# Performance work log

Measured on AMD Instinct MI355X. Metric: run time of the kernel, lower is better.

The kernel has to match this reference:

```python
import jax, jax.numpy as jnp
import numpy as np

B, T, D, H, W = 2, 16, 64, 64, 64
MAX_GROWTH = 0.0  # max_growth_rate init kwarg

def _ln(x, g, b):
    m = x.mean(-1, keepdims=True)
    v = x.var(-1, keepdims=True)
    return (x - m) * jax.lax.rsqrt(v + 1e-5) * g + b

def _pscan(A, X):
    # linear recurrence h_t = A_t*h_{t-1} + X_t via Blelchlo-style associative scan over axis 1
    def comb(l, r):
        a1, x1 = l
        a2, x2 = r
        return a1 * a2, a2 * x1 + x2
    return jax.lax.associative_scan(comb, (A, X), axis=1)[1]

def setup_inputs() -> dict:
    key = jax.random.key(0)
    ks = jax.random.split(key, 20)
    n = lambda k, s, sc=1.0: jax.random.normal(k, s, dtype=jnp.float32) * sc
    inp = dict(
        x_re=n(ks[0], (B, T, D, H, W)), x_im=n(ks[1], (B, T, D, H, W)),
        h_re=n(ks[2], (B * H * W, 1, D)), h_im=n(ks[3], (B * H * W, 1, D)),
        flux_re=n(ks[4], (B, D)), flux_im=n(ks[5], (B, D)),
        dt_seq=0.01 + 0.1 * jax.random.uniform(ks[6], (B, T), dtype=jnp.float32),
        g_s=jnp.ones(2 * D, jnp.float32), b_s=jnp.zeros(2 * D, jnp.float32),
        Wc=n(ks[7], (3, 3, 2 * D, 2 * D), 1.0 / np.sqrt(9 * 2 * D)), bc=jnp.zeros(2 * D, jnp.float32),
        g_t=jnp.ones(2 * D, jnp.float32), b_t=jnp.zeros(2 * D, jnp.float32),
        E_re=n(ks[8], (D, D), 1.0 / np.sqrt(D)), E_im=n(ks[9], (D, D), 1.0 / np.sqrt(D)),
        Dec_re=n(ks[10], (D, D), 1.0 / np.sqrt(D)), Dec_im=n(ks[11], (D, D), 1.0 / np.sqrt(D)),
        lam_flux_raw=jnp.zeros(D, jnp.float32),
        Wsrc_re=n(ks[12], (D, D), 1.0 / np.sqrt(D)), Wsrc_im=n(ks[13], (D, D), 1.0 / np.sqrt(D)),
        w_gate=n(ks[14], (D,)), b_gate=jnp.zeros(D, jnp.float32),
        lam_re_raw=jnp.ones(D, jnp.float32), lam_im=n(ks[15], (D,)),
        W1=n(ks[16], (2 * D, 8 * D), 1.0 / np.sqrt(2 * D)), b1=jnp.zeros(8 * D, jnp.float32),
        W2=n(ks[17], (8 * D, 2 * D), 1.0 / np.sqrt(8 * D)), b2=jnp.zeros(2 * D, jnp.float32),
    )
    return inp

def _forward(x_re, x_im, h_re, h_im, flux_re, flux_im, dt_seq, g_s, b_s, Wc, bc, g_t, b_t,
             E_re, E_im, Dec_re, Dec_im, lam_flux_raw, Wsrc_re, Wsrc_im, w_gate, b_gate,
             lam_re_raw, lam_im, W1, b1, W2, b2):
    # channel-last complex field (B,T,H,W,D)
    x = jnp.moveaxis(x_re, 2, -1) + 1j * jnp.moveaxis(x_im, 2, -1)
    # --- spatial residual branch: LN -> Clifford(= real 2D conv on [re;im] channels) ---
    xr = jnp.concatenate([x.real, x.imag], -1)  # (B,T,H,W,2D)
    xn = _ln(xr, g_s, b_s).reshape(B * T, H, W, 2 * D)
    xs = jax.lax.conv_general_dilated(xn, Wc, (1, 1), 'SAME',
                                      dimension_numbers=('NHWC', 'HWIO', 'NHWC')) + bc
    xs = xs.reshape(B, T, H, W, 2 * D)
    x = x + (xs[..., :D] + 1j * xs[..., D:])
    # --- eigen-basis encode ---
    x_eig = jnp.einsum('bthwd,de->bthwe', x, E_re + 1j * E_im)
    x_mean = x_eig.mean((2, 3))  # (B,T,D)
    # --- flux tracker scan ---
    lam_f = jax.nn.softplus(lam_flux_raw)
    A_flux = jnp.exp(-lam_f * dt_seq[..., None])  # (B,T,D) real decay
    flux = _pscan(A_flux.astype(x_mean.dtype), x_mean * dt_seq[..., None])
    flux = flux + (flux_re + 1j * flux_im)[:, None, :] * jnp.cumprod(A_flux, axis=1)
    source = jnp.einsum('btd,de->bte', flux, Wsrc_re + 1j * Wsrc_im)
    gate = jax.nn.sigmoid(flux.real * w_gate + b_gate)  # real gate in [0,1]
    flux_out = flux[:, -1]
    ge = gate[:, :, None, None, :]
    forcing = x_eig * ge + source[:, :, None, None, :] * (1.0 - ge)
    # --- temporal propagator (exact exponential integrator) ---
    lam = (MAX_GROWTH - jax.nn.softplus(lam_re_raw)) + 1j * lam_im  # Re(lam) <= max_growth_rate
    op_decay = jnp.exp(lam * dt_seq[..., None])            # (B,T,D)
    op_forcing = (op_decay - 1.0) / lam
    u = forcing * op_forcing[:, :, None, None, :]          # (B,T,H,W,D)
    h_prev = (h_re + 1j * h_im).reshape(B, H, W, D)
    u = u.at[:, 0].add(h_prev * op_decay[:, 0][:, None, None, :])
    A_full = jnp.broadcast_to(op_decay[:, :, None, None, :], u.shape)
    u_out = _pscan(A_full, u)                              # (B,T,H,W,D)
    h_out = u_out[:, -1].reshape(B * H * W, 1, D)
    # --- decode + temporal LN/FFN residual ---
    decoded = jnp.einsum('bthwd,de->bthwe', u_out, Dec_re + 1j * Dec_im)
    dn = _ln(jnp.concatenate([decoded.real, decoded.imag], -1), g_t, b_t)
    h1 = jax.nn.gelu(jnp.einsum('bthwc,cf->bthwf', dn, W1) + b1)
    d2 = jnp.einsum('bthwf,fc->bthwc', h1, W2) + b2
    delta = d2[..., :D] + 1j * d2[..., D:]
    z = x + decoded + delta
    return z, h_out, flux_out

def reference(x_re, x_im, h_re, h_im, flux_re, flux_im, dt_seq, g_s, b_s, Wc, bc, g_t, b_t,
              E_re, E_im, Dec_re, Dec_im, lam_flux_raw, Wsrc_re, Wsrc_im, w_gate, b_gate,
              lam_re_raw, lam_im, W1, b1, W2, b2):
    z, h_out, flux_out = _forward(x_re, x_im, h_re, h_im, flux_re, flux_im, dt_seq, g_s, b_s,
                                  Wc, bc, g_t, b_t, E_re, E_im, Dec_re, Dec_im, lam_flux_raw,
                                  Wsrc_re, Wsrc_im, w_gate, b_gate, lam_re_raw, lam_im,
                                  W1, b1, W2, b2)
    # complex outputs returned as real/imag stacked on last axis
    return (jnp.stack([z.real, z.imag], -1),
            jnp.stack([h_out.real, h_out.imag], -1),
            jnp.stack([flux_out.real, flux_out.imag], -1))
```

## Files before the change

### kernel.cpp

```cpp
#include <hip/hip_runtime.h>
#include <hip/hip_bf16.h>


typedef __hip_bfloat16 bf16;
typedef __attribute__((ext_vector_type(8))) short bhalf8;
typedef __attribute__((ext_vector_type(4))) float floatx4;

#define DEV __device__ __forceinline__

DEV float b2f(const bf16 x) { return __bfloat162float(x); }
DEV bf16  f2b(float x)      { return __float2bfloat16(x); }
DEV unsigned short f2bu(float x) { bf16 h = f2b(x); return *(unsigned short*)&h; }
DEV float bu2f(unsigned short u) { unsigned int t = ((unsigned int)u) << 16; return *(float*)&t; }
DEV float softplusf(float x){ return x > 20.f ? x : log1pf(expf(x)); }
DEV float geluf(float x) {
    float v = x * fmaf(x * x, 0.10294324f, 2.30220819f);
    float e = __builtin_amdgcn_exp2f(-v);
    return x * __builtin_amdgcn_rcpf(1.f + e);
}

static constexpr int B_ = 2, T_ = 16, D_ = 64, HW = 4096;
static constexpr int NPIX = B_ * T_ * HW;
static constexpr long long N1 = (long long)NPIX * 128;

static constexpr long long BUFA  = 0;
static constexpr long long XUBF  = N1;
static constexpr long long DECBF = N1 + N1 / 2;
static constexpr long long XNBF  = 2 * N1;
static constexpr long long XCBF  = 2 * N1 + N1 / 2;
static constexpr long long XMEAN = 3 * N1;
static constexpr long long TABS  = XMEAN + 4096;
static constexpr long long FLAGO = TABS + 14336;
static constexpr long long WCP   = FLAGO + 64;
static constexpr long long W1P   = WCP + 73728;
static constexpr long long W2P   = W1P + 32768;
static constexpr long long WEP   = W2P + 32768;
static constexpr long long WDP   = WEP + 8192;

static constexpr long long ZOUT = 0;
static constexpr long long HOUT = 16777216;
static constexpr long long FOUT = 17825792;

DEV float ld(const void* p, long long i, bool bf) {
    if (bf) return b2f(((const bf16*)p)[i]);
    return ((const float*)p)[i];
}

__global__ void k_detect(const unsigned short* __restrict__ x, float* __restrict__ ws) {
    int lane = threadIdx.x;
    int cnt = 0;
    for (int i = lane; i < 256; i += 64) {
        int e = (x[i] >> 7) & 0xFF;
        cnt += (e >= 100 && e <= 140) ? 1 : 0;
    }
    for (int m = 1; m < 64; m <<= 1) cnt += __shfl_xor(cnt, m, 64);
    if (lane == 0) ws[FLAGO] = (cnt >= 224) ? 1.f : 0.f;
}

__global__ void k_convert(const void* Wc, const void* W1, const void* W2,
                          const void* Er, const void* Ei, const void* Dr, const void* Di,
                          float* ws) {
    bool bf = ws[FLAGO] != 0.f;
    int i = blockIdx.x * 256 + threadIdx.x;
    unsigned short* wcp = (unsigned short*)(ws + WCP);
    unsigned short* w1p = (unsigned short*)(ws + W1P);
    unsigned short* w2p = (unsigned short*)(ws + W2P);
    unsigned short* wep = (unsigned short*)(ws + WEP);
    unsigned short* wdp = (unsigned short*)(ws + WDP);
    if (i < 147456) {
        int j = i & 7, lane = (i >> 3) & 63, nt = (i >> 9) & 7, kc = (i >> 12) & 3, tap = i >> 14;
        int ic = kc * 32 + ((lane >> 4) << 3) + j, oc = nt * 16 + (lane & 15);
        wcp[i] = f2bu(ld(Wc, tap * 16384 + ic * 128 + oc, bf)); return;
    } i -= 147456;
    if (i < 65536) {
        int j = i & 7, lane = (i >> 3) & 63, nt = (i >> 9) & 31, kc = i >> 14;
        int ic = kc * 32 + ((lane >> 4) << 3) + j, oc = nt * 16 + (lane & 15);
        w1p[i] = f2bu(ld(W1, ic * 512 + oc, bf)); return;
    } i -= 65536;
    if (i < 65536) {
        int j = i & 7, lane = (i >> 3) & 63, nt = (i >> 9) & 7, kc = i >> 12;
        int ic = kc * 32 + ((lane >> 4) << 3) + j, oc = nt * 16 + (lane & 15);
        w2p[i] = f2bu(ld(W2, ic * 128 + oc, bf)); return;
    } i -= 65536;
    if (i < 16384) {
        int j = i & 7, lane = (i >> 3) & 63, nt = (i >> 9) & 7, kc = i >> 12;
        int k = kc * 32 + ((lane >> 4) << 3) + j, n = nt * 16 + (lane & 15);
        float v;
        if (k < 64) v = (n < 64) ? ld(Er, k * 64 + n, bf) : ld(Ei, k * 64 + (n - 64), bf);
        else        v = (n < 64) ? -ld(Ei, (k - 64) * 64 + n, bf) : ld(Er, (k - 64) * 64 + (n - 64), bf);
        wep[i] = f2bu(v); return;
    } i -= 16384;
    if (i < 16384) {
        int j = i & 7, lane = (i >> 3) & 63, nt = (i >> 9) & 7, kc = i >> 12;
        int k = kc * 32 + ((lane >> 4) << 3) + j, n = nt * 16 + (lane & 15);
        float v;
        if (k < 64) v = (n < 64) ? ld(Dr, k * 64 + n, bf) : ld(Di, k * 64 + (n - 64), bf);
        else        v = (n < 64) ? -ld(Di, (k - 64) * 64 + n, bf) : ld(Dr, (k - 64) * 64 + (n - 64), bf);
        wdp[i] = f2bu(v); return;
    }
}

__global__ __launch_bounds__(256) void kA_ln(const void* __restrict__ xre,
                                             const void* __restrict__ xim,
                                             const void* __restrict__ gs,
                                             const void* __restrict__ bs,
                                             float* __restrict__ ws) {
    __shared__ unsigned short sr[64][72] __attribute__((aligned(16)));
    __shared__ unsigned short si[64][72] __attribute__((aligned(16)));
    __shared__ float red[2][4][64];
    __shared__ float mv[64], rv[64], gb[256];
    bool bf = ws[FLAGO] != 0.f;
    int blk = blockIdx.x;
    int bt = blk >> 6;
    int px0 = (blk & 63) * 64;
    int tid = threadIdx.x;
    gb[tid] = (tid < 128) ? ld(gs, tid, bf) : ld(bs, tid - 128, bf);
    if (bf) {
        const unsigned short* xr16 = (const unsigned short*)xre;
        const unsigned short* xi16 = (const unsigned short*)xim;
        for (int l = tid; l < 1024; l += 256) {
            int a = l >> 9, dd = (l >> 3) & 63, ck = l & 7;
            long long src = (long long)bt * 262144 + (long long)dd * 4096 + px0 + ck * 8;
            bhalf8 v = *(const bhalf8*)&(a ? xi16 : xr16)[src];
            *(bhalf8*)&(a ? si : sr)[dd][ck * 8] = v;
        }
    } else {
        for (int l = tid; l < 8192; l += 256) {
            int a = l >> 12, dd = (l >> 6) & 63, px = l & 63;
            float v = ((const float*)(a ? xim : xre))[(long long)bt * 262144 + (long long)dd * 4096 + px0 + px];
            (a ? si : sr)[dd][px] = f2bu(v);
        }
    }
    __syncthreads();
    int px = tid & 63, part = tid >> 6;
    float s = 0.f, ss = 0.f;
    for (int d = part * 16; d < part * 16 + 16; d++) {
        float r = bu2f(sr[d][px]), q = bu2f(si[d][px]);
        s += r + q; ss += r * r + q * q;
    }
    red[0][part][px] = s; red[1][part][px] = ss;
    __syncthreads();
    if (tid < 64) {
        float S  = red[0][0][tid] + red[0][1][tid] + red[0][2][tid] + red[0][3][tid];
        float SS = red[1][0][tid] + red[1][1][tid] + red[1][2][tid] + red[1][3][tid];
        float m = S * (1.f / 128.f);
        mv[tid] = m;
        rv[tid] = rsqrtf(SS * (1.f / 128.f) - m * m + 1e-5f);
    }
    __syncthreads();
    unsigned short* xcb = (unsigned short*)(ws + XCBF);
    unsigned short* xnb = (unsigned short*)(ws + XNBF);
    long long pbase = ((long long)bt * 4096 + px0) * 128;
    for (int l = tid; l < 8192; l += 256) {
        int p2 = l >> 7, ch = l & 127, d = ch & 63;
        unsigned short raw = (ch < 64 ? sr : si)[d][p2];
        float v = bu2f(raw);
        xcb[pbase + p2 * 128 + ch] = raw;
        xnb[pbase + p2 * 128 + ch] = f2bu((v - mv[p2]) * rv[p2] * gb[ch] + gb[128 + ch]);
    }
}

__global__ __launch_bounds__(256) void kB_conv(const void* __restrict__ bc,
                                               float* __restrict__ ws) {
    __shared__ unsigned short xt[3][64][136] __attribute__((aligned(16)));
    bool bf = ws[FLAGO] != 0.f;
    int blk = blockIdx.x, bt = blk >> 6, h = blk & 63;
    int tid = threadIdx.x, lane = tid & 63, wv = tid >> 6;
    int m16 = lane & 15, quad = lane >> 4;
    const unsigned short* xnb = (const unsigned short*)(ws + XNBF);
    const unsigned short* wcp = (const unsigned short*)(ws + WCP);
    bhalf8 zero8 = {0, 0, 0, 0, 0, 0, 0, 0};
    for (int l = tid; l < 3072; l += 256) {
        int r = l >> 10, rem = l & 1023, col = rem >> 4, ck = rem & 15;
        int hr = h - 1 + r;
        bhalf8 v = zero8;
        if (hr >= 0 && hr < 64)
            v = *(const bhalf8*)&xnb[(((long long)bt * 4096 + hr * 64 + col) << 7) + ck * 8];
        *(bhalf8*)&xt[r][col][ck * 8] = v;
    }
    __syncthreads();
    floatx4 acc[4][2];
    #pragma unroll
    for (int mt = 0; mt < 4; mt++)
        #pragma unroll
        for (int nt = 0; nt < 2; nt++)
            acc[mt][nt] = (floatx4){0.f, 0.f, 0.f, 0.f};
    for (int tap = 0; tap < 9; tap++) {
        int dy = tap / 3, dx = tap - dy * 3;
        #pragma unroll
        for (int kc = 0; kc < 4; kc++) {
            bhalf8 bfr[2];
            #pragma unroll
            for (int nt = 0; nt < 2; nt++)
                bfr[nt] = *(const bhalf8*)&wcp[((((tap * 4 + kc) * 8) + (wv * 2 + nt)) * 64 + lane) * 8];
            #pragma unroll
            for (int mt = 0; mt < 4; mt++) {
                int col = mt * 16 + m16 + dx - 1;
                bhalf8 af = zero8;
                if (col >= 0 && col < 64)
                    af = *(const bhalf8*)&xt[dy][col][kc * 32 + quad * 8];
                acc[mt][0] = __builtin_amdgcn_mfma_f32_16x16x32_bf16(af, bfr[0], acc[mt][0], 0, 0, 0);
                acc[mt][1] = __builtin_amdgcn_mfma_f32_16x16x32_bf16(af, bfr[1], acc[mt][1], 0, 0, 0);
            }
        }
    }
    const unsigned short* xcb = (const unsigned short*)(ws + XCBF);
    unsigned short* xub = (unsigned short*)(ws + XUBF);
    #pragma unroll
    for (int nt = 0; nt < 2; nt++) {
        int n = wv * 32 + nt * 16 + m16;
        float bcv = ld(bc, n, bf);
        #pragma unroll
        for (int mt = 0; mt < 4; mt++)
            #pragma unroll
            for (int r = 0; r < 4; r++) {
                int m = mt * 16 + quad * 4 + r;
                long long p = (long long)bt * 4096 + h * 64 + m;
                xub[p * 128 + n] = f2bu(acc[mt][nt][r] + bu2f(xcb[p * 128 + n]) + bcv);
            }
    }
}

__global__ __launch_bounds__(256) void kC_eig(float* __restrict__ ws) {
    __shared__ unsigned short At[64][136] __attribute__((aligned(16)));
    int blk = blockIdx.x, bt = blk >> 6;
    long long px0 = (long long)blk * 64;
    int tid = threadIdx.x, lane = tid & 63, wv = tid >> 6;
    int m16 = lane & 15, quad = lane >> 4;
    const unsigned short* xub = (const unsigned short*)(ws + XUBF);
    for (int l = tid; l < 1024; l += 256) {
        int p2 = l >> 4, ck = l & 15;
        *(bhalf8*)&At[p2][ck * 8] = *(const bhalf8*)&xub[(px0 + p2) * 128 + ck * 8];
    }
    __syncthreads();
    const unsigned short* wep = (const unsigned short*)(ws + WEP);
    floatx4 acc[4][2];
    #pragma unroll
    for (int mt = 0; mt < 4; mt++)
        #pragma unroll
        for (int nt = 0; nt < 2; nt++)
            acc[mt][nt] = (floatx4){0.f, 0.f, 0.f, 0.f};
    #pragma unroll
    for (int kc = 0; kc < 4; kc++) {
        bhalf8 bfr[2];
        #pragma unroll
        for (int nt = 0; nt < 2; nt++)
            bfr[nt] = *(const bhalf8*)&wep[(((kc * 8) + wv * 2 + nt) * 64 + lane) * 8];
        #pragma unroll
        for (int mt = 0; mt < 4; mt++) {
            bhalf8 af = *(const bhalf8*)&At[mt * 16 + m16][kc * 32 + quad * 8];
            acc[mt][0] = __builtin_amdgcn_mfma_f32_16x16x32_bf16(af, bfr[0], acc[mt][0], 0, 0, 0);
            acc[mt][1] = __builtin_amdgcn_mfma_f32_16x16x32_bf16(af, bfr[1], acc[mt][1], 0, 0, 0);
        }
    }
    unsigned short* xeb = (unsigned short*)(ws + BUFA);
    #pragma unroll
    for (int nt = 0; nt < 2; nt++) {
        int n = wv * 32 + nt * 16 + m16;
        float part = 0.f;
        #pragma unroll
        for (int mt = 0; mt < 4; mt++)
            #pragma unroll
            for (int r = 0; r < 4; r++) {
                int m = mt * 16 + quad * 4 + r;
                xeb[(px0 + m) * 128 + n] = f2bu(acc[mt][nt][r]);
                part += acc[mt][nt][r];
            }
        part += __shfl_xor(part, 16, 64);
        part += __shfl_xor(part, 32, 64);
        if (quad == 0) atomicAdd(ws + XMEAN + bt * 128 + n, part);
    }
}

__global__ __launch_bounds__(256) void kD_flux(const void* __restrict__ fxr, const void* __restrict__ fxi,
                                               const void* __restrict__ dtseq, const void* __restrict__ lamflux,
                                               const void* __restrict__ Wsr, const void* __restrict__ Wsi,
                                               const void* __restrict__ wgate, const void* __restrict__ bgate,
                                               const void* __restrict__ lamreraw, const void* __restrict__ lamim,
                                               float* __restrict__ ws, void* __restrict__ outv) {
    bool bfo = ws[FLAGO] != 0.f;
    int b = blockIdx.x;
    int tid = threadIdx.x;
    int d = tid & 63, g = tid >> 6;
    __shared__ float fr[64], fi[64], psr[4][64], psi[4][64];
    float lam_f = softplusf(ld(lamflux, d, bfo));
    float lre = -softplusf(ld(lamreraw, d, bfo));
    float lim = ld(lamim, d, bfo);
    float cr = 0.f, ci = 0.f;
    if (g == 0) { cr = ld(fxr, b * 64 + d, bfo); ci = ld(fxi, b * 64 + d, bfo); }
    float* tabs = ws + TABS;
    const float* xmean = ws + XMEAN;
    for (int t = 0; t < 16; t++) {
        float dt = ld(dtseq, b * 16 + t, bfo);
        int idx = b * 1024 + t * 64 + d;
        if (g == 0) {
            float A = expf(-lam_f * dt);
            float xr = xmean[(b * 16 + t) * 128 + d]      * (1.f / 4096.f) * dt;
            float xq = xmean[(b * 16 + t) * 128 + 64 + d] * (1.f / 4096.f) * dt;
            cr = A * cr + xr; ci = A * ci + xq;
            fr[d] = cr; fi[d] = ci;
        }
        __syncthreads();
        {
            float pr = 0.f, pi = 0.f;
            #pragma unroll
            for (int k = 0; k < 16; k++) {
                int d2 = g * 16 + k;
                float wr = ld(Wsr, d2 * 64 + d, bfo), wi = ld(Wsi, d2 * 64 + d, bfo);
                pr += fr[d2] * wr - fi[d2] * wi;
                pi += fr[d2] * wi + fi[d2] * wr;
            }
            psr[g][d] = pr; psi[g][d] = pi;
        }
        if (g == 1) {
            float od  = expf(lre * dt);
            float odr = od * cosf(lim * dt);
            float odi = od * sinf(lim * dt);
            tabs[3 * 2048 + idx] = odr; tabs[4 * 2048 + idx] = odi;
            float den = lre * lre + lim * lim;
            float tr = odr - 1.f;
            tabs[5 * 2048 + idx] = (tr * lre + odi * lim) / den;
            tabs[6 * 2048 + idx] = (odi * lre - tr * lim) / den;
        }
        __syncthreads();
        if (g == 0) {
            float sr = psr[0][d] + psr[1][d] + psr[2][d] + psr[3][d];
            float si2 = psi[0][d] + psi[1][d] + psi[2][d] + psi[3][d];
            tabs[1 * 2048 + idx] = sr; tabs[2 * 2048 + idx] = si2;
            tabs[0 * 2048 + idx] = 1.f / (1.f + expf(-(cr * ld(wgate, d, bfo) + ld(bgate, d, bfo))));
            if (t == 15) {
                if (bfo) {
                    bf16* ob = (bf16*)outv;
                    ob[FOUT + (b * 64 + d) * 2]     = f2b(cr);
                    ob[FOUT + (b * 64 + d) * 2 + 1] = f2b(ci);
                } else {
                    float* of = (float*)outv;
                    of[FOUT + (b * 64 + d) * 2]     = cr;
                    of[FOUT + (b * 64 + d) * 2 + 1] = ci;
                }
            }
        }
    }
}

__global__ __launch_bounds__(256) void kE_scan(const void* __restrict__ hre,
                                               const void* __restrict__ him,
                                               float* __restrict__ ws, void* __restrict__ outv) {
    __shared__ float tab[7][16][64];
    bool bfo = ws[FLAGO] != 0.f;
    long long G = (long long)blockIdx.x * 256 + threadIdx.x;
    int d = threadIdx.x & 63;
    int pix = (int)((G >> 6) & 4095);
    int b = (int)(G >> 18);
    const float* tabs = ws + TABS;
    for (int l = threadIdx.x; l < 7 * 1024; l += 256) {
        int a = l >> 10, idx = l & 1023;
        ((float*)tab)[l] = tabs[a * 2048 + b * 1024 + idx];
    }
    __syncthreads();
    long long hidx = ((long long)b * 4096 + pix) * 64 + d;
    float cr = ld(hre, hidx, bfo), ci = ld(him, hidx, bfo);
    const unsigned short* xe = (const unsigned short*)(ws + BUFA);
    unsigned short* ub = (unsigned short*)(ws + XCBF);
    for (int t = 0; t < 16; t++) {
        long long base = ((long long)((b * 16 + t) * 4096 + pix)) * 128 + d;
        float xr = bu2f(xe[base]), xi = bu2f(xe[base + 64]);
        float gt = tab[0][t][d], sr = tab[1][t][d], si = tab[2][t][d];
        float odr = tab[3][t][d], odi = tab[4][t][d];
        float ofr = tab[5][t][d], ofi = tab[6][t][d];
        float fre = xr * gt + sr * (1.f - gt);
        float fim = xi * gt + si * (1.f - gt);
        float ure = fre * ofr - fim * ofi;
        float uim = fre * ofi + fim * ofr;
        float ncr = odr * cr - odi * ci + ure;
        float nci = odr * ci + odi * cr + uim;
        cr = ncr; ci = nci;
        ub[base] = f2bu(cr); ub[base + 64] = f2bu(ci);
    }
    if (bfo) {
        __hip_bfloat162 hv; hv.x = f2b(cr); hv.y = f2b(ci);
        ((__hip_bfloat162*)((bf16*)outv + HOUT))[hidx] = hv;
    } else {
        float2 hv; hv.x = cr; hv.y = ci;
        ((float2*)((float*)outv + HOUT))[hidx] = hv;
    }
}

__global__ __launch_bounds__(256) void kF1_dec(const void* __restrict__ gt_,
                                               const void* __restrict__ bt_,
                                               float* __restrict__ ws) {
    __shared__ unsigned short At[64][136] __attribute__((aligned(16)));
    __shared__ float Ct[64][132];
    __shared__ float mv[64], rv[64], gbt[256];
    bool bf = ws[FLAGO] != 0.f;
    long long px0 = (long long)blockIdx.x * 64;
    int tid = threadIdx.x, lane = tid & 63, wv = tid >> 6;
    int m16 = lane & 15, quad = lane >> 4;
    gbt[tid] = (tid < 128) ? ld(gt_, tid, bf) : ld(bt_, tid - 128, bf);
    const unsigned short* uo = (const unsigned short*)(ws + XCBF);
    for (int l = tid; l < 1024; l += 256) {
        int p2 = l >> 4, ck = l & 15;
        *(bhalf8*)&At[p2][ck * 8] = *(const bhalf8*)&uo[(px0 + p2) * 128 + ck * 8];
    }
    __syncthreads();
    const unsigned short* wdp = (const unsigned short*)(ws + WDP);
    floatx4 acc[4][2];
    #pragma unroll
    for (int mt = 0; mt < 4; mt++)
        #pragma unroll
        for (int nt = 0; nt < 2; nt++)
            acc[mt][nt] = (floatx4){0.f, 0.f, 0.f, 0.f};
    #pragma unroll
    for (int kc = 0; kc < 4; kc++) {
        bhalf8 bfr[2];
        #pragma unroll
        for (int nt = 0; nt < 2; nt++)
            bfr[nt] = *(const bhalf8*)&wdp[(((kc * 8) + wv * 2 + nt) * 64 + lane) * 8];
        #pragma unroll
        for (int mt = 0; mt < 4; mt++) {
            bhalf8 af = *(const bhalf8*)&At[mt * 16 + m16][kc * 32 + quad * 8];
            acc[mt][0] = __builtin_amdgcn_mfma_f32_16x16x32_bf16(af, bfr[0], acc[mt][0], 0, 0, 0);
            acc[mt][1] = __builtin_amdgcn_mfma_f32_16x16x32_bf16(af, bfr[1], acc[mt][1], 0, 0, 0);
        }
    }
    #pragma unroll
    for (int nt = 0; nt < 2; nt++) {
        int n = wv * 32 + nt * 16 + m16;
        #pragma unroll
        for (int mt = 0; mt < 4; mt++)
            #pragma unroll
            for (int r = 0; r < 4; r++)
                Ct[mt * 16 + quad * 4 + r][n] = acc[mt][nt][r];
    }
    __syncthreads();
    if (tid < 64) {
        float s = 0.f, ss = 0.f;
        for (int ch = 0; ch < 128; ch++) { float v = Ct[tid][ch]; s += v; ss += v * v; }
        float m = s * (1.f / 128.f);
        mv[tid] = m;
        rv[tid] = rsqrtf(ss * (1.f / 128.f) - m * m + 1e-5f);
    }
    __syncthreads();
    unsigned short* decb = (unsigned short*)(ws + DECBF);
    unsigned short* dnb  = (unsigned short*)(ws + XNBF);
    for (int l = tid; l < 8192; l += 256) {
        int p2 = l >> 7, ch = l & 127;
        float v = Ct[p2][ch];
        decb[(px0 + p2) * 128 + ch] = f2bu(v);
        dnb [(px0 + p2) * 128 + ch] = f2bu((v - mv[p2]) * rv[p2] * gbt[ch] + gbt[128 + ch]);
    }
}

__global__ __launch_bounds__(256, 5) void kMLP(const void* __restrict__ b1v,
                                               const void* __restrict__ b2v,
                                               float* __restrict__ ws, void* __restrict__ outv) {
    __shared__ unsigned short A1[32][136] __attribute__((aligned(16)));
    __shared__ unsigned short h1f[8][2][64][8] __attribute__((aligned(16)));
    __shared__ float gb2[128];
    bool bf = ws[FLAGO] != 0.f;
    long long px0 = (long long)blockIdx.x * 32;
    int tid = threadIdx.x, lane = tid & 63, wv = tid >> 6;
    int m16 = lane & 15, quad = lane >> 4;
    const unsigned short* dnb = (const unsigned short*)(ws + XNBF);
    if (tid < 128) gb2[tid] = ld(b2v, tid, bf);
    for (int l = tid; l < 512; l += 256) {
        int p2 = l >> 4, ck = l & 15;
        *(bhalf8*)&A1[p2][ck * 8] = *(const bhalf8*)&dnb[(px0 + p2) * 128 + ck * 8];
    }
    __syncthreads();
    const unsigned short* w1p = (const unsigned short*)(ws + W1P);
    const unsigned short* w2p = (const unsigned short*)(ws + W2P);
    floatx4 acc2[2][2];
    #pragma unroll
    for (int mt = 0; mt < 2; mt++)
        #pragma unroll
        for (int nt = 0; nt < 2; nt++)
            acc2[mt][nt] = (floatx4){0.f, 0.f, 0.f, 0.f};

    #pragma unroll
    for (int ph = 0; ph < 2; ph++) {
        floatx4 acc1[2][4];
        #pragma unroll
        for (int mt = 0; mt < 2; mt++)
            #pragma unroll
            for (int nt4 = 0; nt4 < 4; nt4++)
                acc1[mt][nt4] = (floatx4){0.f, 0.f, 0.f, 0.f};
        #pragma unroll
        for (int kc = 0; kc < 4; kc++) {
            bhalf8 af0 = *(const bhalf8*)&A1[m16][kc * 32 + quad * 8];
            bhalf8 af1 = *(const bhalf8*)&A1[16 + m16][kc * 32 + quad * 8];
            #pragma unroll
            for (int nt4 = 0; nt4 < 4; nt4++) {
                int nt = ph * 4 + nt4;
                bhalf8 bfr = *(const bhalf8*)&w1p[(((kc * 32) + wv * 8 + nt) * 64 + lane) * 8];
                acc1[0][nt4] = __builtin_amdgcn_mfma_f32_16x16x32_bf16(af0, bfr, acc1[0][nt4], 0, 0, 0);
                acc1[1][nt4] = __builtin_amdgcn_mfma_f32_16x16x32_bf16(af1, bfr, acc1[1][nt4], 0, 0, 0);
            }
        }
        #pragma unroll
        for (int nt4 = 0; nt4 < 4; nt4++) {
            int nt = ph * 4 + nt4;
            int n = (wv * 8 + nt) * 16 + m16;
            float b1f = ld(b1v, n, bf);
            int qp = ((nt * 2) + (m16 >> 3)) & 3;
            int slot = wv * 2 + (nt4 >> 1);
            int j = m16 & 7;
            #pragma unroll
            for (int mt = 0; mt < 2; mt++)
                #pragma unroll
                for (int r = 0; r < 4; r++)
                    h1f[slot][mt][qp * 16 + quad * 4 + r][j] =
                        f2bu(geluf(acc1[mt][nt4][r] + b1f));
        }
        __syncthreads();
        #pragma unroll
        for (int s = 0; s < 8; s++) {
            int kc2g = (s >> 1) * 4 + (s & 1) + ph * 2;
            bhalf8 a0 = *(const bhalf8*)&h1f[s][0][lane][0];
            bhalf8 a1 = *(const bhalf8*)&h1f[s][1][lane][0];
            #pragma unroll
            for (int nt = 0; nt < 2; nt++) {
                bhalf8 bfr = *(const bhalf8*)&w2p[(((kc2g * 8) + wv * 2 + nt) * 64 + lane) * 8];
                acc2[0][nt] = __builtin_amdgcn_mfma_f32_16x16x32_bf16(a0, bfr, acc2[0][nt], 0, 0, 0);
                acc2[1][nt] = __builtin_amdgcn_mfma_f32_16x16x32_bf16(a1, bfr, acc2[1][nt], 0, 0, 0);
            }
        }
        if (ph == 0) __syncthreads();
    }
    #pragma unroll
    for (int nt = 0; nt < 2; nt++) {
        int n = wv * 32 + nt * 16 + m16;
        #pragma unroll
        for (int mt = 0; mt < 2; mt++)
            #pragma unroll
            for (int r = 0; r < 4; r++)
                A1[mt * 16 + quad * 4 + r][n] = f2bu(acc2[mt][nt][r]);
    }
    __syncthreads();
    {
        const unsigned short* decb = (const unsigned short*)(ws + DECBF);
        const unsigned short* xub  = (const unsigned short*)(ws + XUBF);
        int pxl = tid >> 3, dc = (tid & 7) * 8;
        long long p = px0 + pxl;
        bhalf8 cre = *(const bhalf8*)&A1[pxl][dc];
        bhalf8 cim = *(const bhalf8*)&A1[pxl][64 + dc];
        bhalf8 xr8 = *(const bhalf8*)&xub[p * 128 + dc];
        bhalf8 xi8 = *(const bhalf8*)&xub[p * 128 + 64 + dc];
        bhalf8 dr8 = *(const bhalf8*)&decb[p * 128 + dc];
        bhalf8 di8 = *(const bhalf8*)&decb[p * 128 + 64 + dc];
        float zr[8], zi[8];
        #pragma unroll
        for (int k = 0; k < 8; k++) {
            zr[k] = bu2f((unsigned short)cre[k]) + gb2[dc + k]
                  + bu2f((unsigned short)xr8[k]) + bu2f((unsigned short)dr8[k]);
            zi[k] = bu2f((unsigned short)cim[k]) + gb2[64 + dc + k]
                  + bu2f((unsigned short)xi8[k]) + bu2f((unsigned short)di8[k]);
        }
        if (bf) {
            unsigned short o[16];
            #pragma unroll
            for (int k = 0; k < 8; k++) { o[2 * k] = f2bu(zr[k]); o[2 * k + 1] = f2bu(zi[k]); }
            unsigned short* ob = (unsigned short*)outv;
            *(bhalf8*)&ob[ZOUT + p * 128 + 2 * dc]     = *(bhalf8*)&o[0];
            *(bhalf8*)&ob[ZOUT + p * 128 + 2 * dc + 8] = *(bhalf8*)&o[8];
        } else {
            float* of = (float*)outv + ZOUT + p * 128 + 2 * dc;
            #pragma unroll
            for (int k = 0; k < 8; k++) { of[2 * k] = zr[k]; of[2 * k + 1] = zi[k]; }
        }
    }
}

extern "C" void kernel_launch(void* const* d_in, const int* in_sizes, int n_in,
                              void* d_out, int out_size, void* d_ws, size_t ws_size,
                              hipStream_t stream) {
    const void* x_re  = d_in[0];
    const void* x_im  = d_in[1];
    const void* h_re  = d_in[2];
    const void* h_im  = d_in[3];
    const void* fl_re = d_in[4];
    const void* fl_im = d_in[5];
    const void* dtseq = d_in[6];
    const void* g_s   = d_in[7];
    const void* b_s   = d_in[8];
    const void* Wc    = d_in[9];
    const void* bc    = d_in[10];
    const void* g_t   = d_in[11];
    const void* b_t   = d_in[12];
    const void* E_re  = d_in[13];
    const void* E_im  = d_in[14];
    const void* De_re = d_in[15];
    const void* De_im = d_in[16];
    const void* lamfl = d_in[17];
    const void* Ws_re = d_in[18];
    const void* Ws_im = d_in[19];
    const void* wgate = d_in[20];
    const void* bgate = d_in[21];
    const void* lamrr = d_in[22];
    const void* lamim = d_in[23];
    const void* W1    = d_in[24];
    const void* b1    = d_in[25];
    const void* W2    = d_in[26];
    const void* b2    = d_in[27];
    float* ws = (float*)d_ws;

    hipMemsetAsync((char*)d_ws + XMEAN * sizeof(float), 0, 4096 * sizeof(float), stream);
    k_detect<<<1, 64, 0, stream>>>((const unsigned short*)x_re, ws);
    k_convert<<<1216, 256, 0, stream>>>(Wc, W1, W2, E_re, E_im, De_re, De_im, ws);
    kA_ln<<<2048, 256, 0, stream>>>(x_re, x_im, g_s, b_s, ws);
    kB_conv<<<2048, 256, 0, stream>>>(bc, ws);
    kC_eig<<<2048, 256, 0, stream>>>(ws);
    kD_flux<<<2, 256, 0, stream>>>(fl_re, fl_im, dtseq, lamfl, Ws_re, Ws_im,
                                   wgate, bgate, lamrr, lamim, ws, d_out);
    kE_scan<<<2048, 256, 0, stream>>>(h_re, h_im, ws, d_out);
    kF1_dec<<<2048, 256, 0, stream>>>(g_t, b_t, ws);
    kMLP<<<4096, 256, 0, stream>>>(b1, b2, ws, d_out);
}
```

Before: 450.3 us.

## Fuse eig projection into conv kernel and decoder+LN into MLP kernel

Folds the E-projection GEMM into the conv kernel, reusing the conv output tile from shared memory rather than reloading it from global memory. The decoder GEMM and its LayerNorm move into the MLP kernel, so the decoded and normalized intermediates are no longer written to and read back from global memory. The scan kernel now processes two channels per thread with packed loads and stores, which halves its grid. In exchange, shared-memory pressure rises: the MLP kernel aliases buffers in a pool and needs extra barriers, and its occupancy hint drops from 5 to 4.

```diff
diff --git a/kernel.cpp b/kernel.cpp
--- a/kernel.cpp
+++ b/kernel.cpp
@@ -204,6 +204,8 @@
             }
         }
     }
+    __syncthreads();
+    unsigned short (*At)[136] = (unsigned short(*)[136])&xt[0][0][0];
     const unsigned short* xcb = (const unsigned short*)(ws + XCBF);
     unsigned short* xub = (unsigned short*)(ws + XUBF);
     #pragma unroll
@@ -216,30 +218,20 @@
             for (int r = 0; r < 4; r++) {
                 int m = mt * 16 + quad * 4 + r;
                 long long p = (long long)bt * 4096 + h * 64 + m;
-                xub[p * 128 + n] = f2bu(acc[mt][nt][r] + bu2f(xcb[p * 128 + n]) + bcv);
-            }
-    }
-}
-
-__global__ __launch_bounds__(256) void kC_eig(float* __restrict__ ws) {
-    __shared__ unsigned short At[64][136] __attribute__((aligned(16)));
-    int blk = blockIdx.x, bt = blk >> 6;
+                unsigned short u = f2bu(acc[mt][nt][r] + bu2f(xcb[p * 128 + n]) + bcv);
+                xub[p * 128 + n] = u;
+                At[m][n] = u;
+            }
+    }
+    __syncthreads();
+    const unsigned short* wep = (const unsigned short*)(ws + WEP);
     long long px0 = (long long)blk * 64;
-    int tid = threadIdx.x, lane = tid & 63, wv = tid >> 6;
-    int m16 = lane & 15, quad = lane >> 4;
-    const unsigned short* xub = (const unsigned short*)(ws + XUBF);
-    for (int l = tid; l < 1024; l += 256) {
-        int p2 = l >> 4, ck = l & 15;
-        *(bhalf8*)&At[p2][ck * 8] = *(const bhalf8*)&xub[(px0 + p2) * 128 + ck * 8];
-    }
-    __syncthreads();
-    const unsigned short* wep = (const unsigned short*)(ws + WEP);
-    floatx4 acc[4][2];
+    floatx4 acce[4][2];
     #pragma unroll
     for (int mt = 0; mt < 4; mt++)
         #pragma unroll
         for (int nt = 0; nt < 2; nt++)
-            acc[mt][nt] = (floatx4){0.f, 0.f, 0.f, 0.f};
+            acce[mt][nt] = (floatx4){0.f, 0.f, 0.f, 0.f};
     #pragma unroll
     for (int kc = 0; kc < 4; kc++) {
         bhalf8 bfr[2];
@@ -249,8 +241,8 @@
         #pragma unroll
         for (int mt = 0; mt < 4; mt++) {
             bhalf8 af = *(const bhalf8*)&At[mt * 16 + m16][kc * 32 + quad * 8];
-            acc[mt][0] = __builtin_amdgcn_mfma_f32_16x16x32_bf16(af, bfr[0], acc[mt][0], 0, 0, 0);
-            acc[mt][1] = __builtin_amdgcn_mfma_f32_16x16x32_bf16(af, bfr[1], acc[mt][1], 0, 0, 0);
+            acce[mt][0] = __builtin_amdgcn_mfma_f32_16x16x32_bf16(af, bfr[0], acce[mt][0], 0, 0, 0);
+            acce[mt][1] = __builtin_amdgcn_mfma_f32_16x16x32_bf16(af, bfr[1], acce[mt][1], 0, 0, 0);
         }
     }
     unsigned short* xeb = (unsigned short*)(ws + BUFA);
@@ -263,8 +255,8 @@
             #pragma unroll
             for (int r = 0; r < 4; r++) {
                 int m = mt * 16 + quad * 4 + r;
-                xeb[(px0 + m) * 128 + n] = f2bu(acc[mt][nt][r]);
-                part += acc[mt][nt][r];
+                xeb[(px0 + m) * 128 + n] = f2bu(acce[mt][nt][r]);
+                part += acce[mt][nt][r];
             }
         part += __shfl_xor(part, 16, 64);
         part += __shfl_xor(part, 32, 64);
@@ -348,125 +340,160 @@
                                                float* __restrict__ ws, void* __restrict__ outv) {
     __shared__ float tab[7][16][64];
     bool bfo = ws[FLAGO] != 0.f;
-    long long G = (long long)blockIdx.x * 256 + threadIdx.x;
-    int d = threadIdx.x & 63;
-    int pix = (int)((G >> 6) & 4095);
-    int b = (int)(G >> 18);
+    int tid = threadIdx.x;
+    long long G = (long long)blockIdx.x * 256 + tid;
+    int d0 = (int)(G & 31) * 2;
+    int pixg = (int)(G >> 5);
+    int pix = pixg & 4095;
+    int b = pixg >> 12;
     const float* tabs = ws + TABS;
-    for (int l = threadIdx.x; l < 7 * 1024; l += 256) {
+    for (int l = tid; l < 7 * 1024; l += 256) {
         int a = l >> 10, idx = l & 1023;
         ((float*)tab)[l] = tabs[a * 2048 + b * 1024 + idx];
     }
     __syncthreads();
-    long long hidx = ((long long)b * 4096 + pix) * 64 + d;
-    float cr = ld(hre, hidx, bfo), ci = ld(him, hidx, bfo);
+    long long hidx = ((long long)b * 4096 + pix) * 64 + d0;
+    float cr0, ci0, cr1, ci1;
+    if (bfo) {
+        unsigned int r2 = *(const unsigned int*)&((const unsigned short*)hre)[hidx];
+        unsigned int i2 = *(const unsigned int*)&((const unsigned short*)him)[hidx];
+        cr0 = bu2f((unsigned short)(r2 & 0xffff)); cr1 = bu2f((unsigned short)(r2 >> 16));
+        ci0 = bu2f((unsigned short)(i2 & 0xffff)); ci1 = bu2f((unsigned short)(i2 >> 16));
+    } else {
+        float2 r2 = *(const float2*)((const float*)hre + hidx);
+        float2 i2 = *(const float2*)((const float*)him + hidx);
+        cr0 = r2.x; cr1 = r2.y; ci0 = i2.x; ci1 = i2.y;
+    }
     const unsigned short* xe = (const unsigned short*)(ws + BUFA);
     unsigned short* ub = (unsigned short*)(ws + XCBF);
     for (int t = 0; t < 16; t++) {
-        long long base = ((long long)((b * 16 + t) * 4096 + pix)) * 128 + d;
-        float xr = bu2f(xe[base]), xi = bu2f(xe[base + 64]);
-        float gt = tab[0][t][d], sr = tab[1][t][d], si = tab[2][t][d];
-        float odr = tab[3][t][d], odi = tab[4][t][d];
-        float ofr = tab[5][t][d], ofi = tab[6][t][d];
-        float fre = xr * gt + sr * (1.f - gt);
-        float fim = xi * gt + si * (1.f - gt);
-        float ure = fre * ofr - fim * ofi;
-        float uim = fre * ofi + fim * ofr;
-        float ncr = odr * cr - odi * ci + ure;
-        float nci = odr * ci + odi * cr + uim;
-        cr = ncr; ci = nci;
-        ub[base] = f2bu(cr); ub[base + 64] = f2bu(ci);
+        long long base = ((long long)((b * 16 + t) * 4096 + pix)) * 128 + d0;
+        unsigned int xr2 = *(const unsigned int*)&xe[base];
+        unsigned int xi2 = *(const unsigned int*)&xe[base + 64];
+        float2 gt2  = *(const float2*)&tab[0][t][d0];
+        float2 sr2  = *(const float2*)&tab[1][t][d0];
+        float2 si2  = *(const float2*)&tab[2][t][d0];
+        float2 odr2 = *(const float2*)&tab[3][t][d0];
+        float2 odi2 = *(const float2*)&tab[4][t][d0];
+        float2 ofr2 = *(const float2*)&tab[5][t][d0];
+        float2 ofi2 = *(const float2*)&tab[6][t][d0];
+        {
+            float xr = bu2f((unsigned short)(xr2 & 0xffff));
+            float xi = bu2f((unsigned short)(xi2 & 0xffff));
+            float fre = xr * gt2.x + sr2.x * (1.f - gt2.x);
+            float fim = xi * gt2.x + si2.x * (1.f - gt2.x);
+            float ure = fre * ofr2.x - fim * ofi2.x;
+            float uim = fre * ofi2.x + fim * ofr2.x;
+            float n0 = odr2.x * cr0 - odi2.x * ci0 + ure;
+            float n1 = odr2.x * ci0 + odi2.x * cr0 + uim;
+            cr0 = n0; ci0 = n1;
+        }
+        {
+            float xr = bu2f((unsigned short)(xr2 >> 16));
+            float xi = bu2f((unsigned short)(xi2 >> 16));
+            float fre = xr * gt2.y + sr2.y * (1.f - gt2.y);
+            float fim = xi * gt2.y + si2.y * (1.f - gt2.y);
+            float ure = fre * ofr2.y - fim * ofi2.y;
+            float uim = fre * ofi2.y + fim * ofr2.y;
+            float n0 = odr2.y * cr1 - odi2.y * ci1 + ure;
+            float n1 = odr2.y * ci1 + odi2.y * cr1 + uim;
+            cr1 = n0; ci1 = n1;
+        }
+        *(unsigned int*)&ub[base]      = (unsigned int)f2bu(cr0) | ((unsigned int)f2bu(cr1) << 16);
+        *(unsigned int*)&ub[base + 64] = (unsigned int)f2bu(ci0) | ((unsigned int)f2bu(ci1) << 16);
     }
     if (bfo) {
-        __hip_bfloat162 hv; hv.x = f2b(cr); hv.y = f2b(ci);
-        ((__hip_bfloat162*)((bf16*)outv + HOUT))[hidx] = hv;
+        uint2 hv;
+        hv.x = (unsigned int)f2bu(cr0) | ((unsigned int)f2bu(ci0) << 16);
+        hv.y = (unsigned int)f2bu(cr1) | ((unsigned int)f2bu(ci1) << 16);
+        *(uint2*)((unsigned short*)outv + HOUT + 2 * hidx) = hv;
     } else {
-        float2 hv; hv.x = cr; hv.y = ci;
-        ((float2*)((float*)outv + HOUT))[hidx] = hv;
-    }
-}
-
-__global__ __launch_bounds__(256) void kF1_dec(const void* __restrict__ gt_,
+        float4 hv; hv.x = cr0; hv.y = ci0; hv.z = cr1; hv.w = ci1;
+        *(float4*)((float*)outv + HOUT + 2 * hidx) = hv;
+    }
+}
+
+__global__ __launch_bounds__(256, 4) void kMLP(const void* __restrict__ gt_,
                                                const void* __restrict__ bt_,
-                                               float* __restrict__ ws) {
-    __shared__ unsigned short At[64][136] __attribute__((aligned(16)));
-    __shared__ float Ct[64][132];
-    __shared__ float mv[64], rv[64], gbt[256];
-    bool bf = ws[FLAGO] != 0.f;
-    long long px0 = (long long)blockIdx.x * 64;
-    int tid = threadIdx.x, lane = tid & 63, wv = tid >> 6;
-    int m16 = lane & 15, quad = lane >> 4;
-    gbt[tid] = (tid < 128) ? ld(gt_, tid, bf) : ld(bt_, tid - 128, bf);
-    const unsigned short* uo = (const unsigned short*)(ws + XCBF);
-    for (int l = tid; l < 1024; l += 256) {
-        int p2 = l >> 4, ck = l & 15;
-        *(bhalf8*)&At[p2][ck * 8] = *(const bhalf8*)&uo[(px0 + p2) * 128 + ck * 8];
-    }
-    __syncthreads();
-    const unsigned short* wdp = (const unsigned short*)(ws + WDP);
-    floatx4 acc[4][2];
-    #pragma unroll
-    for (int mt = 0; mt < 4; mt++)
-        #pragma unroll
-        for (int nt = 0; nt < 2; nt++)
-            acc[mt][nt] = (floatx4){0.f, 0.f, 0.f, 0.f};
-    #pragma unroll
-    for (int kc = 0; kc < 4; kc++) {
-        bhalf8 bfr[2];
-        #pragma unroll
-        for (int nt = 0; nt < 2; nt++)
-            bfr[nt] = *(const bhalf8*)&wdp[(((kc * 8) + wv * 2 + nt) * 64 + lane) * 8];
-        #pragma unroll
-        for (int mt = 0; mt < 4; mt++) {
-            bhalf8 af = *(const bhalf8*)&At[mt * 16 + m16][kc * 32 + quad * 8];
-            acc[mt][0] = __builtin_amdgcn_mfma_f32_16x16x32_bf16(af, bfr[0], acc[mt][0], 0, 0, 0);
-            acc[mt][1] = __builtin_amdgcn_mfma_f32_16x16x32_bf16(af, bfr[1], acc[mt][1], 0, 0, 0);
-        }
-    }
-    #pragma unroll
-    for (int nt = 0; nt < 2; nt++) {
-        int n = wv * 32 + nt * 16 + m16;
-        #pragma unroll
-        for (int mt = 0; mt < 4; mt++)
-            #pragma unroll
-            for (int r = 0; r < 4; r++)
-                Ct[mt * 16 + quad * 4 + r][n] = acc[mt][nt][r];
-    }
-    __syncthreads();
-    if (tid < 64) {
-        float s = 0.f, ss = 0.f;
-        for (int ch = 0; ch < 128; ch++) { float v = Ct[tid][ch]; s += v; ss += v * v; }
-        float m = s * (1.f / 128.f);
-        mv[tid] = m;
-        rv[tid] = rsqrtf(ss * (1.f / 128.f) - m * m + 1e-5f);
-    }
-    __syncthreads();
-    unsigned short* decb = (unsigned short*)(ws + DECBF);
-    unsigned short* dnb  = (unsigned short*)(ws + XNBF);
-    for (int l = tid; l < 8192; l += 256) {
-        int p2 = l >> 7, ch = l & 127;
-        float v = Ct[p2][ch];
-        decb[(px0 + p2) * 128 + ch] = f2bu(v);
-        dnb [(px0 + p2) * 128 + ch] = f2bu((v - mv[p2]) * rv[p2] * gbt[ch] + gbt[128 + ch]);
-    }
-}
-
-__global__ __launch_bounds__(256, 5) void kMLP(const void* __restrict__ b1v,
+                                               const void* __restrict__ b1v,
                                                const void* __restrict__ b2v,
                                                float* __restrict__ ws, void* __restrict__ outv) {
+    __shared__ unsigned char POOL[16384] __attribute__((aligned(16)));
+    __shared__ unsigned short Dt[32][136] __attribute__((aligned(16)));
     __shared__ unsigned short A1[32][136] __attribute__((aligned(16)));
-    __shared__ unsigned short h1f[8][2][64][8] __attribute__((aligned(16)));
+    __shared__ float gbt[256];
     __shared__ float gb2[128];
+    __shared__ float psS[4][32], psQ[4][32];
+    __shared__ float mvv[32], rvv[32];
+    unsigned short (*UA)[136] = (unsigned short(*)[136])POOL;
+    unsigned short (*h1f)[2][64][8] = (unsigned short(*)[2][64][8])POOL;
     bool bf = ws[FLAGO] != 0.f;
     long long px0 = (long long)blockIdx.x * 32;
     int tid = threadIdx.x, lane = tid & 63, wv = tid >> 6;
     int m16 = lane & 15, quad = lane >> 4;
-    const unsigned short* dnb = (const unsigned short*)(ws + XNBF);
+    gbt[tid] = (tid < 128) ? ld(gt_, tid, bf) : ld(bt_, tid - 128, bf);
     if (tid < 128) gb2[tid] = ld(b2v, tid, bf);
+    const unsigned short* uo = (const unsigned short*)(ws + XCBF);
     for (int l = tid; l < 512; l += 256) {
         int p2 = l >> 4, ck = l & 15;
-        *(bhalf8*)&A1[p2][ck * 8] = *(const bhalf8*)&dnb[(px0 + p2) * 128 + ck * 8];
-    }
+        *(bhalf8*)&UA[p2][ck * 8] = *(const bhalf8*)&uo[(px0 + p2) * 128 + ck * 8];
+    }
+    __syncthreads();
+    const unsigned short* wdp = (const unsigned short*)(ws + WDP);
+    floatx4 accd[2][2];
+    #pragma unroll
+    for (int mt = 0; mt < 2; mt++)
+        #pragma unroll
+        for (int nt = 0; nt < 2; nt++)
+            accd[mt][nt] = (floatx4){0.f, 0.f, 0.f, 0.f};
+    #pragma unroll
+    for (int kc = 0; kc < 4; kc++) {
+        bhalf8 bfr0 = *(const bhalf8*)&wdp[(((kc * 8) + wv * 2 + 0) * 64 + lane) * 8];
+        bhalf8 bfr1 = *(const bhalf8*)&wdp[(((kc * 8) + wv * 2 + 1) * 64 + lane) * 8];
+        bhalf8 af0 = *(const bhalf8*)&UA[m16][kc * 32 + quad * 8];
+        bhalf8 af1 = *(const bhalf8*)&UA[16 + m16][kc * 32 + quad * 8];
+        accd[0][0] = __builtin_amdgcn_mfma_f32_16x16x32_bf16(af0, bfr0, accd[0][0], 0, 0, 0);
+        accd[0][1] = __builtin_amdgcn_mfma_f32_16x16x32_bf16(af0, bfr1, accd[0][1], 0, 0, 0);
+        accd[1][0] = __builtin_amdgcn_mfma_f32_16x16x32_bf16(af1, bfr0, accd[1][0], 0, 0, 0);
+        accd[1][1] = __builtin_amdgcn_mfma_f32_16x16x32_bf16(af1, bfr1, accd[1][1], 0, 0, 0);
+    }
+    #pragma unroll
+    for (int mt = 0; mt < 2; mt++)
+        #pragma unroll
+        for (int r = 0; r < 4; r++) {
+            int mrow = mt * 16 + quad * 4 + r;
+            float a0 = accd[mt][0][r], a1 = accd[mt][1][r];
+            Dt[mrow][wv * 32 + m16]      = f2bu(a0);
+            Dt[mrow][wv * 32 + 16 + m16] = f2bu(a1);
+            float s = a0 + a1, q = a0 * a0 + a1 * a1;
+            #pragma unroll
+            for (int msk = 1; msk <= 8; msk <<= 1) {
+                s += __shfl_xor(s, msk, 64);
+                q += __shfl_xor(q, msk, 64);
+            }
+            if (m16 == 0) { psS[wv][mrow] = s; psQ[wv][mrow] = q; }
+        }
+    __syncthreads();
+    if (tid < 32) {
+        float S = psS[0][tid] + psS[1][tid] + psS[2][tid] + psS[3][tid];
+        float Q = psQ[0][tid] + psQ[1][tid] + psQ[2][tid] + psQ[3][tid];
+        float m = S * (1.f / 128.f);
+        mvv[tid] = m;
+        rvv[tid] = rsqrtf(Q * (1.f / 128.f) - m * m + 1e-5f);
+    }
+    __syncthreads();
+    #pragma unroll
+    for (int mt = 0; mt < 2; mt++)
+        #pragma unroll
+        for (int r = 0; r < 4; r++) {
+            int mrow = mt * 16 + quad * 4 + r;
+            float mu = mvv[mrow], rs = rvv[mrow];
+            #pragma unroll
+            for (int nt = 0; nt < 2; nt++) {
+                int n = wv * 32 + nt * 16 + m16;
+                A1[mrow][n] = f2bu((accd[mt][nt][r] - mu) * rs * gbt[n] + gbt[128 + n]);
+            }
+        }
     __syncthreads();
     const unsigned short* w1p = (const unsigned short*)(ws + W1P);
     const unsigned short* w2p = (const unsigned short*)(ws + W2P);
@@ -476,7 +503,6 @@
         #pragma unroll
         for (int nt = 0; nt < 2; nt++)
             acc2[mt][nt] = (floatx4){0.f, 0.f, 0.f, 0.f};
-
     #pragma unroll
     for (int ph = 0; ph < 2; ph++) {
         floatx4 acc1[2][4];
@@ -497,6 +523,7 @@
                 acc1[1][nt4] = __builtin_amdgcn_mfma_f32_16x16x32_bf16(af1, bfr, acc1[1][nt4], 0, 0, 0);
             }
         }
+        if (ph == 0) __syncthreads();
         #pragma unroll
         for (int nt4 = 0; nt4 < 4; nt4++) {
             int nt = ph * 4 + nt4;
@@ -538,16 +565,15 @@
     }
     __syncthreads();
     {
-        const unsigned short* decb = (const unsigned short*)(ws + DECBF);
-        const unsigned short* xub  = (const unsigned short*)(ws + XUBF);
+        const unsigned short* xub = (const unsigned short*)(ws + XUBF);
         int pxl = tid >> 3, dc = (tid & 7) * 8;
         long long p = px0 + pxl;
         bhalf8 cre = *(const bhalf8*)&A1[pxl][dc];
         bhalf8 cim = *(const bhalf8*)&A1[pxl][64 + dc];
         bhalf8 xr8 = *(const bhalf8*)&xub[p * 128 + dc];
         bhalf8 xi8 = *(const bhalf8*)&xub[p * 128 + 64 + dc];
-        bhalf8 dr8 = *(const bhalf8*)&decb[p * 128 + dc];
-        bhalf8 di8 = *(const bhalf8*)&decb[p * 128 + 64 + dc];
+        bhalf8 dr8 = *(const bhalf8*)&Dt[pxl][dc];
+        bhalf8 di8 = *(const bhalf8*)&Dt[pxl][64 + dc];
         float zr[8], zi[8];
         #pragma unroll
         for (int k = 0; k < 8; k++) {
@@ -609,10 +635,8 @@
     k_convert<<<1216, 256, 0, stream>>>(Wc, W1, W2, E_re, E_im, De_re, De_im, ws);
     kA_ln<<<2048, 256, 0, stream>>>(x_re, x_im, g_s, b_s, ws);
     kB_conv<<<2048, 256, 0, stream>>>(bc, ws);
-    kC_eig<<<2048, 256, 0, stream>>>(ws);
     kD_flux<<<2, 256, 0, stream>>>(fl_re, fl_im, dtseq, lamfl, Ws_re, Ws_im,
                                    wgate, bgate, lamrr, lamim, ws, d_out);
-    kE_scan<<<2048, 256, 0, stream>>>(h_re, h_im, ws, d_out);
-    kF1_dec<<<2048, 256, 0, stream>>>(g_t, b_t, ws);
-    kMLP<<<4096, 256, 0, stream>>>(b1, b2, ws, d_out);
-}
+    kE_scan<<<1024, 256, 0, stream>>>(h_re, h_im, ws, d_out);
+    kMLP<<<4096, 256, 0, stream>>>(g_t, b_t, b1, b2, ws, d_out);
+}
```

New measurement: 414.9 us. 1.09x faster.
